# Kernel optimization log

Hardware: AMD Instinct MI355X
Metric: run time of the kernel (lower is better)

## Reference

```python
import jax, jax.numpy as jnp
import numpy as np

BS, S, DM, H = 4, 512, 512, 8
DK = DM // H
EPS = 1e-6


def setup_inputs() -> dict:
    key = jax.random.key(0)
    ks = jax.random.split(key, 11)
    sc = jnp.float32(0.02)  # small init so exp(q @ k^T) stays finite (no max-subtraction in original)
    return {
        "q": jax.random.normal(ks[0], (BS, S, DM), jnp.float32),
        "k": jax.random.normal(ks[1], (BS, S, DM), jnp.float32),
        "v": jax.random.normal(ks[2], (BS, S, DM), jnp.float32),
        "Wq": sc * jax.random.normal(ks[3], (DM, DM), jnp.float32),
        "bq": jnp.zeros((DM,), jnp.float32),
        "Wk": sc * jax.random.normal(ks[4], (DM, DM), jnp.float32),
        "bk": jnp.zeros((DM,), jnp.float32),
        "Wv": sc * jax.random.normal(ks[5], (DM, DM), jnp.float32),
        "bv": jnp.zeros((DM,), jnp.float32),
        "Wo": sc * jax.random.normal(ks[6], (DM, DM), jnp.float32),
        "bo": jnp.zeros((DM,), jnp.float32),
        "alpha": jnp.ones((DK,), jnp.float32),   # Norm.alpha over last dim (= d_k per head)
        "beta": jnp.zeros((DK,), jnp.float32),   # Norm.bias
    }


def reference(q, k, v, Wq, bq, Wk, bk, Wv, bv, Wo, bo, alpha, beta):
    # project and split heads: [bs, h, s, d_k]
    qh = (q @ Wq + bq).reshape(BS, S, H, DK).transpose(0, 2, 1, 3)
    kh = (k @ Wk + bk).reshape(BS, S, H, DK).transpose(0, 2, 1, 3)
    vh = (v @ Wv + bv).reshape(BS, S, H, DK).transpose(0, 2, 1, 3)

    # pairwise-batch exp scores: E[bq, bk, h, i, j] = exp(q[bq] @ k[bk]^T)
    E = jnp.exp(jnp.einsum('bhid,chjd->bchij', qh, kh))  # [BS, BS, H, S, S]
    # fenmu: sum over k-batch, each term scaled by sqrt(d_k) (as in original loop)
    fenmu = jnp.sqrt(jnp.float32(DK)) * E.sum(axis=1)     # [BS, H, S, S]
    # fenzi: same-batch exp scores (diagonal of pairwise tensor)
    fenzi = E[jnp.arange(BS), jnp.arange(BS)]             # [BS, H, S, S]
    R = fenzi / fenmu                                     # [BS, H, S, S]

    # per v-batch-entry score: score[bq, c] = R[bq] @ v[c]
    score = jnp.einsum('bhij,chjd->bchid', R, vh)         # [BS, BS, H, S, DK]
    sm = jax.nn.softmax(score, axis=-1)
    # Norm: torch.std is unbiased (ddof=1); eps added to std, not variance
    mu = sm.mean(axis=-1, keepdims=True)
    std = jnp.sqrt(sm.var(axis=-1, ddof=1, keepdims=True))
    ln = alpha * (sm - mu) / (std + EPS) + beta

    # output += LN(score) + q, accumulated over the v-batch loop (BS iterations)
    heads = ln.sum(axis=1) + jnp.float32(BS) * qh         # [BS, H, S, DK]
    concat = heads.transpose(0, 2, 1, 3).reshape(BS, S, DM)
    return concat @ Wo + bo
```

## Files before the change

### kernel.cpp

```cpp
#include <hip/hip_runtime.h>
#include <hip/hip_bf16.h>

#define BSZ 4
#define SEQ 512
#define DMODEL 512
#define NHEAD 8
#define DKH 64
#define EPSLN 1e-6f

typedef short bf16x8 __attribute__((ext_vector_type(8)));
typedef float f32x4 __attribute__((ext_vector_type(4)));

static __device__ __forceinline__ short f2bf(float x) {
  unsigned u = __builtin_bit_cast(unsigned, x);
  u = (u + 0x7FFFu + ((u >> 16) & 1u)) >> 16;
  return (short)u;
}
static __device__ __forceinline__ bf16x8 cvt8(float4 a, float4 b) {
  bf16x8 r;
  r[0] = f2bf(a.x); r[1] = f2bf(a.y); r[2] = f2bf(a.z); r[3] = f2bf(a.w);
  r[4] = f2bf(b.x); r[5] = f2bf(b.y); r[6] = f2bf(b.z); r[7] = f2bf(b.w);
  return r;
}
static __device__ __forceinline__ unsigned pk2(float a, float b) {
  return (unsigned)(unsigned short)f2bf(a) |
         ((unsigned)(unsigned short)f2bf(b) << 16);
}
static __device__ __forceinline__ void async_cp16(const void* g, void* l) {
  __builtin_amdgcn_global_load_lds(
      (const __attribute__((address_space(1))) unsigned int*)g,
      (__attribute__((address_space(3))) unsigned int*)l, 16, 0, 0);
}

__global__ __launch_bounds__(256) void cast3_kernel(
    const float* __restrict__ q, const float* __restrict__ k,
    const float* __restrict__ v, short* __restrict__ qb,
    short* __restrict__ kb, short* __restrict__ vb) {
  const float* s; short* d;
  switch (blockIdx.y) {
    case 0: s = q; d = qb; break;
    case 1: s = k; d = kb; break;
    default: s = v; d = vb; break;
  }
  const size_t idx = (size_t)blockIdx.x * 2048 + (size_t)threadIdx.x * 8;
  float4 a = *(const float4*)&s[idx];
  float4 b = *(const float4*)&s[idx + 4];
  *(bf16x8*)&d[idx] = cvt8(a, b);
}

__global__ __launch_bounds__(256) void wcast_kernel(
    const float* __restrict__ Wq, const float* __restrict__ Wk,
    const float* __restrict__ Wv, const float* __restrict__ Wo,
    short* __restrict__ Wqt, short* __restrict__ Wkt,
    short* __restrict__ Wvt, short* __restrict__ Wot) {
  __shared__ float T[64][65];
  const float* src; short* dst;
  switch (blockIdx.z) {
    case 0: src = Wq; dst = Wqt; break;
    case 1: src = Wk; dst = Wkt; break;
    case 2: src = Wv; dst = Wvt; break;
    default: src = Wo; dst = Wot; break;
  }
  const int k0 = blockIdx.x * 64, n0 = blockIdx.y * 64;
  const int tid = threadIdx.x;
  const int n4 = (tid & 15) * 4, kk = tid >> 4;
#pragma unroll
  for (int p = 0; p < 4; ++p) {
    float4 v = *(const float4*)&src[(size_t)(k0 + kk + p * 16) * DMODEL + n0 + n4];
    T[kk + p * 16][n4 + 0] = v.x;
    T[kk + p * 16][n4 + 1] = v.y;
    T[kk + p * 16][n4 + 2] = v.z;
    T[kk + p * 16][n4 + 3] = v.w;
  }
  __syncthreads();
  const int k4 = (tid & 15) * 4;
#pragma unroll
  for (int p = 0; p < 4; ++p) {
    const int nn = (tid >> 4) + p * 16;
    float x0 = T[k4 + 0][nn], x1 = T[k4 + 1][nn];
    float x2 = T[k4 + 2][nn], x3 = T[k4 + 3][nn];
    uint2 u; u.x = pk2(x0, x1); u.y = pk2(x2, x3);
    *(uint2*)&dst[(size_t)(n0 + nn) * DMODEL + k0 + k4] = u;
  }
}

__device__ __forceinline__ void gemm_body(
    const short* __restrict__ A, const short* __restrict__ Wt,
    const float* __restrict__ bias, void* __restrict__ out, int omode) {
  __shared__ short As[2][128 * 32];
  __shared__ short Bs[2][128 * 32];
  const int tid = threadIdx.x;
  const int w = tid >> 6, lane = tid & 63;
  const int l15 = lane & 15, q = lane >> 4;
  const int wm = w >> 1, wn = w & 1;
  const int bn = blockIdx.x * 128, bm = blockIdx.y * 128;
  const int wu = __builtin_amdgcn_readfirstlane(w);
  const int srow = wu * 16 + (lane >> 2);
  const int sch = lane & 3;

  f32x4 acc[4][4] = {};

#define GSTAGE(k0, buf)                                                      \
  {                                                                          \
    const short* ga0 = A + (size_t)(bm + srow) * 512 + (k0) + sch * 8;       \
    const short* ga1 = A + (size_t)(bm + srow + 64) * 512 + (k0) + sch * 8;  \
    const short* gb0 = Wt + (size_t)(bn + srow) * 512 + (k0) + sch * 8;      \
    const short* gb1 = Wt + (size_t)(bn + srow + 64) * 512 + (k0) + sch * 8; \
    async_cp16(ga0, &As[buf][wu * 512]);                                     \
    async_cp16(ga1, &As[buf][(4 + wu) * 512]);                               \
    async_cp16(gb0, &Bs[buf][wu * 512]);                                     \
    async_cp16(gb1, &Bs[buf][(4 + wu) * 512]);                               \
  }

  GSTAGE(0, 0);
  for (int ks = 0; ks < 16; ++ks) {
    __syncthreads();
    if (ks < 15) GSTAGE((ks + 1) * 32, (ks + 1) & 1);
    const short* a = As[ks & 1];
    const short* bsh = Bs[ks & 1];
    bf16x8 af[4], bfr[4];
#pragma unroll
    for (int mt = 0; mt < 4; ++mt)
      af[mt] = *(const bf16x8*)&a[(wm * 64 + mt * 16 + l15) * 32 + q * 8];
#pragma unroll
    for (int nt = 0; nt < 4; ++nt)
      bfr[nt] = *(const bf16x8*)&bsh[(wn * 64 + nt * 16 + l15) * 32 + q * 8];
#pragma unroll
    for (int mt = 0; mt < 4; ++mt)
#pragma unroll
      for (int nt = 0; nt < 4; ++nt)
        acc[mt][nt] = __builtin_amdgcn_mfma_f32_16x16x32_bf16(
            af[mt], bfr[nt], acc[mt][nt], 0, 0, 0);
  }
#undef GSTAGE

  float bv[4];
#pragma unroll
  for (int nt = 0; nt < 4; ++nt) bv[nt] = bias[bn + wn * 64 + nt * 16 + l15];
#pragma unroll
  for (int mt = 0; mt < 4; ++mt)
#pragma unroll
    for (int nt = 0; nt < 4; ++nt) {
      const int col = bn + wn * 64 + nt * 16 + l15;
#pragma unroll
      for (int r = 0; r < 4; ++r) {
        const int row = bm + wm * 64 + mt * 16 + q * 4 + r;
        const float val = acc[mt][nt][r] + bv[nt];
        if (omode == 0) {
          ((float*)out)[(size_t)row * 512 + col] = val;
        } else if (omode == 1) {
          ((short*)out)[(size_t)row * 512 + col] = f2bf(val);
        } else {
          const int cc = row >> 9, j = row & 511;
          const int hh = col >> 6, d = col & 63;
          ((short*)out)[(((size_t)(cc * 8 + hh) * 64 + d) << 9) + j] = f2bf(val);
        }
      }
    }
}

__global__ __launch_bounds__(256, 2) void proj_gemm(
    const short* qb, const short* kb, const short* vb,
    const short* Wqt, const short* Wkt, const short* Wvt,
    const float* bq, const float* bk, const float* bvs,
    float* Qp, short* Kb, short* Vt) {
  const short* A; const short* Wt; const float* bias; void* out; int omode;
  switch (blockIdx.z) {
    case 0: A = qb; Wt = Wqt; bias = bq; out = Qp; omode = 0; break;
    case 1: A = kb; Wt = Wkt; bias = bk; out = Kb; omode = 1; break;
    default: A = vb; Wt = Wvt; bias = bvs; out = Vt; omode = 2; break;
  }
  gemm_body(A, Wt, bias, out, omode);
}

__global__ __launch_bounds__(256, 2) void out_gemm(
    const short* Hc, const short* Wot, const float* bo, float* out) {
  gemm_body(Hc, Wot, bo, out, 0);
}

__global__ __launch_bounds__(256, 3) void attn2_kernel(
    const float* __restrict__ Qp, const short* __restrict__ Kb,
    const short* __restrict__ Vt, const float* __restrict__ alpha,
    const float* __restrict__ beta, short* __restrict__ Hc) {
  __shared__ __align__(16) short Stage[2][64 * 64];
  __shared__ __align__(16) short Rs[32][72];
  __shared__ __align__(16) float xch[16 * 128];

  const int it = blockIdx.x, h = blockIdx.y, b = blockIdx.z;
  const int i0 = it * 32;
  const int tid = threadIdx.x;
  const int w = tid >> 6, lane = tid & 63;
  const int l15 = lane & 15, q = lane >> 4;
  const int wi = w >> 1, wj = w & 1;
  const int wu = __builtin_amdgcn_readfirstlane(w);

  const float* qrow =
      Qp + (size_t)(b * SEQ + i0 + wi * 16 + l15) * DMODEL + h * DKH;
  const bf16x8 aq0 = cvt8(*(const float4*)(qrow + q * 8),
                          *(const float4*)(qrow + q * 8 + 4));
  const bf16x8 aq1 = cvt8(*(const float4*)(qrow + 32 + q * 8),
                          *(const float4*)(qrow + 32 + q * 8 + 4));

  const int srow0 = wu * 8 + (lane >> 3);
  const int scol = (lane & 7) ^ (lane >> 3);

  const short* kbase_h = Kb + h * DKH;
  const short* vbase_h = Vt + (((size_t)h * DKH) << 9);

#define STG(g0, rstride, buf)                                             \
  {                                                                       \
    async_cp16((g0) + (size_t)srow0 * (rstride) + scol * 8,               \
               &Stage[buf][wu * 512]);                                    \
    async_cp16((g0) + (size_t)(srow0 + 32) * (rstride) + scol * 8,        \
               &Stage[buf][(4 + wu) * 512]);                              \
  }

  f32x4 acc[4][4] = {};
  float sacc[2][4], ebb[2][4];

  STG(kbase_h, DMODEL, 0);

  for (int jt = 0; jt < 8; ++jt) {
    const int j0 = jt * 64;
    bf16x8 ar;
#pragma unroll
    for (int ph = 0; ph < 8; ++ph) {
      __syncthreads();
      const int buf = ph & 1, nbuf = buf ^ 1;
      if (ph < 3) {
        STG(kbase_h + ((size_t)((ph + 1) * SEQ) + j0) * DMODEL, DMODEL, nbuf);
      } else if (ph < 7) {
        const int cn = ph - 3;
        STG(vbase_h + (((size_t)(cn * NHEAD * DKH)) << 9) + j0, SEQ, nbuf);
      } else if (jt < 7) {
        STG(kbase_h + (size_t)(j0 + 64) * DMODEL, DMODEL, nbuf);
      }
      const short* S = Stage[buf];
      if (ph < 4) {
        if (ph == 0) {
#pragma unroll
          for (int t = 0; t < 2; ++t)
#pragma unroll
            for (int r = 0; r < 4; ++r) sacc[t][r] = 0.0f;
        }
#pragma unroll
        for (int ntl = 0; ntl < 2; ++ntl) {
          const int row = (wj * 2 + ntl) * 16 + l15;
          const int p0 = q ^ (l15 & 7);
          bf16x8 b0 = *(const bf16x8*)&S[row * 64 + p0 * 8];
          bf16x8 b1 = *(const bf16x8*)&S[row * 64 + (p0 ^ 4) * 8];
          f32x4 s = {};
          s = __builtin_amdgcn_mfma_f32_16x16x32_bf16(aq0, b0, s, 0, 0, 0);
          s = __builtin_amdgcn_mfma_f32_16x16x32_bf16(aq1, b1, s, 0, 0, 0);
#pragma unroll
          for (int r = 0; r < 4; ++r) {
            const float e = __expf(s[r]);
            sacc[ntl][r] += e;
            if (ph == b) ebb[ntl][r] = e;
          }
        }
        if (ph == 3) {
#pragma unroll
          for (int ntl = 0; ntl < 2; ++ntl)
#pragma unroll
            for (int r = 0; r < 4; ++r)
              Rs[wi * 16 + q * 4 + r][(wj * 2 + ntl) * 16 + l15] =
                  f2bf(ebb[ntl][r] / (8.0f * sacc[ntl][r]));
        }
      } else {
        if (ph == 4) ar = *(const bf16x8*)&Rs[wi * 16 + l15][wj * 32 + q * 8];
#pragma unroll
        for (int nt = 0; nt < 4; ++nt) {
          const int row = nt * 16 + l15;
          const int pb = (wj * 4 + q) ^ (l15 & 7);
          bf16x8 bv = *(const bf16x8*)&S[row * 64 + pb * 8];
          acc[ph - 4][nt] = __builtin_amdgcn_mfma_f32_16x16x32_bf16(
              ar, bv, acc[ph - 4][nt], 0, 0, 0);
        }
      }
    }
  }
#undef STG

#pragma unroll
  for (int c = 0; c < BSZ; ++c) {
    if (wj == 1) {
#pragma unroll
      for (int nt = 0; nt < 4; ++nt)
#pragma unroll
        for (int r = 0; r < 4; ++r)
          xch[(nt * 4 + r) * 128 + wi * 64 + lane] = acc[c][nt][r];
    }
    __syncthreads();
    if (wj == 0) {
#pragma unroll
      for (int nt = 0; nt < 4; ++nt)
#pragma unroll
        for (int r = 0; r < 4; ++r)
          acc[c][nt][r] += xch[(nt * 4 + r) * 128 + wi * 64 + lane];
    }
    __syncthreads();
  }

  if (wj == 0) {
    float al[4], be[4];
#pragma unroll
    for (int nt = 0; nt < 4; ++nt) {
      al[nt] = alpha[nt * 16 + l15];
      be[nt] = beta[nt * 16 + l15];
    }
    float hacc[4][4] = {};
#pragma unroll
    for (int c = 0; c < BSZ; ++c) {
#pragma unroll
      for (int r = 0; r < 4; ++r) {
        float e0 = __expf(acc[c][0][r]), e1 = __expf(acc[c][1][r]);
        float e2 = __expf(acc[c][2][r]), e3 = __expf(acc[c][3][r]);
        float es = e0 + e1 + e2 + e3;
#pragma unroll
        for (int m = 8; m >= 1; m >>= 1) es += __shfl_xor(es, m);
        const float inv = 1.0f / es;
        const float d0 = e0 * inv - 0.015625f, d1 = e1 * inv - 0.015625f;
        const float d2 = e2 * inv - 0.015625f, d3 = e3 * inv - 0.015625f;
        float sq = d0 * d0 + d1 * d1 + d2 * d2 + d3 * d3;
#pragma unroll
        for (int m = 8; m >= 1; m >>= 1) sq += __shfl_xor(sq, m);
        const float rs = 1.0f / (sqrtf(sq * (1.0f / 63.0f)) + EPSLN);
        hacc[r][0] += al[0] * d0 * rs + be[0];
        hacc[r][1] += al[1] * d1 * rs + be[1];
        hacc[r][2] += al[2] * d2 * rs + be[2];
        hacc[r][3] += al[3] * d3 * rs + be[3];
      }
    }
#pragma unroll
    for (int r = 0; r < 4; ++r) {
      const size_t rowoff =
          (size_t)(b * SEQ + i0 + wi * 16 + q * 4 + r) * DMODEL + h * DKH;
#pragma unroll
      for (int nt = 0; nt < 4; ++nt) {
        const int d = nt * 16 + l15;
        const float o = hacc[r][nt] + 4.0f * Qp[rowoff + d];
        Hc[rowoff + d] = f2bf(o);
      }
    }
  }
}

extern "C" void kernel_launch(void* const* d_in, const int* in_sizes, int n_in,
                              void* d_out, int out_size, void* d_ws,
                              size_t ws_size, hipStream_t stream) {
  (void)in_sizes; (void)n_in; (void)out_size; (void)ws_size;
  const float* q = (const float*)d_in[0];
  const float* k = (const float*)d_in[1];
  const float* v = (const float*)d_in[2];
  const float* Wq = (const float*)d_in[3];
  const float* bq = (const float*)d_in[4];
  const float* Wk = (const float*)d_in[5];
  const float* bk = (const float*)d_in[6];
  const float* Wv = (const float*)d_in[7];
  const float* bv = (const float*)d_in[8];
  const float* Wo = (const float*)d_in[9];
  const float* bo = (const float*)d_in[10];
  const float* alpha = (const float*)d_in[11];
  const float* beta = (const float*)d_in[12];
  float* out = (float*)d_out;

  char* wsb = (char*)d_ws;
  short* qb = (short*)(wsb);
  short* kb = (short*)(wsb + (2u << 20));
  short* vb = (short*)(wsb + (4u << 20));
  float* Qp = (float*)(wsb + (6u << 20));
  short* Kb = (short*)(wsb + (10u << 20));
  short* Vtg = (short*)(wsb + (12u << 20));
  short* Hc = (short*)(wsb + (14u << 20));
  short* Wqt = (short*)(wsb + (16u << 20));
  short* Wkt = (short*)(wsb + (16u << 20) + (512u << 10));
  short* Wvt = (short*)(wsb + (17u << 20));
  short* Wot = (short*)(wsb + (17u << 20) + (512u << 10));

  cast3_kernel<<<dim3(512, 3), 256, 0, stream>>>(q, k, v, qb, kb, vb);
  wcast_kernel<<<dim3(8, 8, 4), 256, 0, stream>>>(Wq, Wk, Wv, Wo,
                                                  Wqt, Wkt, Wvt, Wot);
  proj_gemm<<<dim3(4, 16, 3), 256, 0, stream>>>(qb, kb, vb, Wqt, Wkt, Wvt,
                                                bq, bk, bv, Qp, Kb, Vtg);
  attn2_kernel<<<dim3(16, 8, 4), 256, 0, stream>>>(Qp, Kb, Vtg, alpha, beta,
                                                   Hc);
  out_gemm<<<dim3(4, 16), 256, 0, stream>>>(Hc, Wot, bo, out);
}
```

Measured before the change: 161.0 us.

## Merge cast kernels and stage two K/V tiles per barrier in attention

The activation cast and weight transpose-cast kernels become one launch, dispatched by block index, which saves a kernel launch. In the attention kernel each pipeline phase now loads and consumes two 64x64 tiles instead of one. That halves the number of __syncthreads per j-tile, from 8 to 4, and doubles the staging LDS. The larger LDS footprint may lower occupancy under the 3-blocks-per-CU launch bound.

```diff
diff --git a/kernel.cpp b/kernel.cpp
--- a/kernel.cpp
+++ b/kernel.cpp
@@ -32,45 +32,49 @@
       (__attribute__((address_space(3))) unsigned int*)l, 16, 0, 0);
 }
 
-__global__ __launch_bounds__(256) void cast3_kernel(
+__global__ __launch_bounds__(256) void prep_kernel(
     const float* __restrict__ q, const float* __restrict__ k,
     const float* __restrict__ v, short* __restrict__ qb,
-    short* __restrict__ kb, short* __restrict__ vb) {
-  const float* s; short* d;
-  switch (blockIdx.y) {
-    case 0: s = q; d = qb; break;
-    case 1: s = k; d = kb; break;
-    default: s = v; d = vb; break;
-  }
-  const size_t idx = (size_t)blockIdx.x * 2048 + (size_t)threadIdx.x * 8;
-  float4 a = *(const float4*)&s[idx];
-  float4 b = *(const float4*)&s[idx + 4];
-  *(bf16x8*)&d[idx] = cvt8(a, b);
-}
-
-__global__ __launch_bounds__(256) void wcast_kernel(
+    short* __restrict__ kb, short* __restrict__ vb,
     const float* __restrict__ Wq, const float* __restrict__ Wk,
     const float* __restrict__ Wv, const float* __restrict__ Wo,
     short* __restrict__ Wqt, short* __restrict__ Wkt,
     short* __restrict__ Wvt, short* __restrict__ Wot) {
   __shared__ float T[64][65];
+  const int bx = blockIdx.x;
+  if (bx < 1536) {
+    const int which = bx >> 9, blk = bx & 511;
+    const float* s; short* d;
+    switch (which) {
+      case 0: s = q; d = qb; break;
+      case 1: s = k; d = kb; break;
+      default: s = v; d = vb; break;
+    }
+    const size_t idx = (size_t)blk * 2048 + (size_t)threadIdx.x * 8;
+    float4 a = *(const float4*)&s[idx];
+    float4 b = *(const float4*)&s[idx + 4];
+    *(bf16x8*)&d[idx] = cvt8(a, b);
+    return;
+  }
+  const int r = bx - 1536;
+  const int mat = r >> 6, m = r & 63;
+  const int k0 = (m & 7) * 64, n0 = (m >> 3) * 64;
   const float* src; short* dst;
-  switch (blockIdx.z) {
+  switch (mat) {
     case 0: src = Wq; dst = Wqt; break;
     case 1: src = Wk; dst = Wkt; break;
     case 2: src = Wv; dst = Wvt; break;
     default: src = Wo; dst = Wot; break;
   }
-  const int k0 = blockIdx.x * 64, n0 = blockIdx.y * 64;
   const int tid = threadIdx.x;
   const int n4 = (tid & 15) * 4, kk = tid >> 4;
 #pragma unroll
   for (int p = 0; p < 4; ++p) {
-    float4 v = *(const float4*)&src[(size_t)(k0 + kk + p * 16) * DMODEL + n0 + n4];
-    T[kk + p * 16][n4 + 0] = v.x;
-    T[kk + p * 16][n4 + 1] = v.y;
-    T[kk + p * 16][n4 + 2] = v.z;
-    T[kk + p * 16][n4 + 3] = v.w;
+    float4 w4 = *(const float4*)&src[(size_t)(k0 + kk + p * 16) * DMODEL + n0 + n4];
+    T[kk + p * 16][n4 + 0] = w4.x;
+    T[kk + p * 16][n4 + 1] = w4.y;
+    T[kk + p * 16][n4 + 2] = w4.z;
+    T[kk + p * 16][n4 + 3] = w4.w;
   }
   __syncthreads();
   const int k4 = (tid & 15) * 4;
@@ -182,7 +186,7 @@
     const float* __restrict__ Qp, const short* __restrict__ Kb,
     const short* __restrict__ Vt, const float* __restrict__ alpha,
     const float* __restrict__ beta, short* __restrict__ Hc) {
-  __shared__ __align__(16) short Stage[2][64 * 64];
+  __shared__ __align__(16) short Stage[2][2 * 4096];
   __shared__ __align__(16) short Rs[32][72];
   __shared__ __align__(16) float xch[16 * 128];
 
@@ -207,59 +211,71 @@
   const short* kbase_h = Kb + h * DKH;
   const short* vbase_h = Vt + (((size_t)h * DKH) << 9);
 
-#define STG(g0, rstride, buf)                                             \
+#define STG1(g0, rs, buf, tslot)                                          \
   {                                                                       \
-    async_cp16((g0) + (size_t)srow0 * (rstride) + scol * 8,               \
-               &Stage[buf][wu * 512]);                                    \
-    async_cp16((g0) + (size_t)(srow0 + 32) * (rstride) + scol * 8,        \
-               &Stage[buf][(4 + wu) * 512]);                              \
-  }
+    async_cp16((g0) + (size_t)srow0 * (rs) + scol * 8,                    \
+               &Stage[buf][(tslot) * 4096 + wu * 512]);                   \
+    async_cp16((g0) + (size_t)(srow0 + 32) * (rs) + scol * 8,             \
+               &Stage[buf][(tslot) * 4096 + (4 + wu) * 512]);             \
+  }
+#define KTILE(c, j0) (kbase_h + ((size_t)((c) * SEQ) + (j0)) * DMODEL)
+#define VTILE(c, j0) (vbase_h + (((size_t)((c) * NHEAD * DKH)) << 9) + (j0))
 
   f32x4 acc[4][4] = {};
   float sacc[2][4], ebb[2][4];
 
-  STG(kbase_h, DMODEL, 0);
+  STG1(KTILE(0, 0), DMODEL, 0, 0);
+  STG1(KTILE(1, 0), DMODEL, 0, 1);
 
   for (int jt = 0; jt < 8; ++jt) {
     const int j0 = jt * 64;
     bf16x8 ar;
 #pragma unroll
-    for (int ph = 0; ph < 8; ++ph) {
+    for (int ph2 = 0; ph2 < 4; ++ph2) {
       __syncthreads();
-      const int buf = ph & 1, nbuf = buf ^ 1;
-      if (ph < 3) {
-        STG(kbase_h + ((size_t)((ph + 1) * SEQ) + j0) * DMODEL, DMODEL, nbuf);
-      } else if (ph < 7) {
-        const int cn = ph - 3;
-        STG(vbase_h + (((size_t)(cn * NHEAD * DKH)) << 9) + j0, SEQ, nbuf);
+      const int buf = ph2 & 1, nbuf = buf ^ 1;
+      if (ph2 == 0) {
+        STG1(KTILE(2, j0), DMODEL, nbuf, 0);
+        STG1(KTILE(3, j0), DMODEL, nbuf, 1);
+      } else if (ph2 == 1) {
+        STG1(VTILE(0, j0), SEQ, nbuf, 0);
+        STG1(VTILE(1, j0), SEQ, nbuf, 1);
+      } else if (ph2 == 2) {
+        STG1(VTILE(2, j0), SEQ, nbuf, 0);
+        STG1(VTILE(3, j0), SEQ, nbuf, 1);
       } else if (jt < 7) {
-        STG(kbase_h + (size_t)(j0 + 64) * DMODEL, DMODEL, nbuf);
+        STG1(KTILE(0, j0 + 64), DMODEL, nbuf, 0);
+        STG1(KTILE(1, j0 + 64), DMODEL, nbuf, 1);
       }
-      const short* S = Stage[buf];
-      if (ph < 4) {
-        if (ph == 0) {
+      if (ph2 < 2) {
+        if (ph2 == 0) {
 #pragma unroll
           for (int t = 0; t < 2; ++t)
 #pragma unroll
-            for (int r = 0; r < 4; ++r) sacc[t][r] = 0.0f;
+            for (int r = 0; r < 4; ++r) { sacc[t][r] = 0.0f; ebb[t][r] = 0.0f; }
         }
 #pragma unroll
-        for (int ntl = 0; ntl < 2; ++ntl) {
-          const int row = (wj * 2 + ntl) * 16 + l15;
-          const int p0 = q ^ (l15 & 7);
-          bf16x8 b0 = *(const bf16x8*)&S[row * 64 + p0 * 8];
-          bf16x8 b1 = *(const bf16x8*)&S[row * 64 + (p0 ^ 4) * 8];
-          f32x4 s = {};
-          s = __builtin_amdgcn_mfma_f32_16x16x32_bf16(aq0, b0, s, 0, 0, 0);
-          s = __builtin_amdgcn_mfma_f32_16x16x32_bf16(aq1, b1, s, 0, 0, 0);
-#pragma unroll
-          for (int r = 0; r < 4; ++r) {
-            const float e = __expf(s[r]);
-            sacc[ntl][r] += e;
-            if (ph == b) ebb[ntl][r] = e;
+        for (int ct = 0; ct < 2; ++ct) {
+          const int c = ph2 * 2 + ct;
+          const short* S = &Stage[buf][ct * 4096];
+#pragma unroll
+          for (int ntl = 0; ntl < 2; ++ntl) {
+            const int row = (wj * 2 + ntl) * 16 + l15;
+            const int p0 = q ^ (l15 & 7);
+            bf16x8 b0 = *(const bf16x8*)&S[row * 64 + p0 * 8];
+            bf16x8 b1 = *(const bf16x8*)&S[row * 64 + (p0 ^ 4) * 8];
+            f32x4 s = {};
+            s = __builtin_amdgcn_mfma_f32_16x16x32_bf16(aq0, b0, s, 0, 0, 0);
+            s = __builtin_amdgcn_mfma_f32_16x16x32_bf16(aq1, b1, s, 0, 0, 0);
+#pragma unroll
+            for (int r = 0; r < 4; ++r) {
+              const float e = __expf(s[r]);
+              sacc[ntl][r] += e;
+              ebb[ntl][r] = (c == b) ? e : ebb[ntl][r];
+            }
           }
         }
-        if (ph == 3) {
+        if (ph2 == 1) {
 #pragma unroll
           for (int ntl = 0; ntl < 2; ++ntl)
 #pragma unroll
@@ -268,19 +284,26 @@
                   f2bf(ebb[ntl][r] / (8.0f * sacc[ntl][r]));
         }
       } else {
-        if (ph == 4) ar = *(const bf16x8*)&Rs[wi * 16 + l15][wj * 32 + q * 8];
-#pragma unroll
-        for (int nt = 0; nt < 4; ++nt) {
-          const int row = nt * 16 + l15;
-          const int pb = (wj * 4 + q) ^ (l15 & 7);
-          bf16x8 bv = *(const bf16x8*)&S[row * 64 + pb * 8];
-          acc[ph - 4][nt] = __builtin_amdgcn_mfma_f32_16x16x32_bf16(
-              ar, bv, acc[ph - 4][nt], 0, 0, 0);
+        if (ph2 == 2) ar = *(const bf16x8*)&Rs[wi * 16 + l15][wj * 32 + q * 8];
+#pragma unroll
+        for (int ct = 0; ct < 2; ++ct) {
+          const int c = (ph2 - 2) * 2 + ct;
+          const short* S = &Stage[buf][ct * 4096];
+#pragma unroll
+          for (int nt = 0; nt < 4; ++nt) {
+            const int row = nt * 16 + l15;
+            const int pb = (wj * 4 + q) ^ (l15 & 7);
+            bf16x8 bv = *(const bf16x8*)&S[row * 64 + pb * 8];
+            acc[c][nt] = __builtin_amdgcn_mfma_f32_16x16x32_bf16(
+                ar, bv, acc[c][nt], 0, 0, 0);
+          }
         }
       }
     }
   }
-#undef STG
+#undef STG1
+#undef KTILE
+#undef VTILE
 
 #pragma unroll
   for (int c = 0; c < BSZ; ++c) {
@@ -378,9 +401,9 @@
   short* Wvt = (short*)(wsb + (17u << 20));
   short* Wot = (short*)(wsb + (17u << 20) + (512u << 10));
 
-  cast3_kernel<<<dim3(512, 3), 256, 0, stream>>>(q, k, v, qb, kb, vb);
-  wcast_kernel<<<dim3(8, 8, 4), 256, 0, stream>>>(Wq, Wk, Wv, Wo,
-                                                  Wqt, Wkt, Wvt, Wot);
+  prep_kernel<<<dim3(1792), 256, 0, stream>>>(q, k, v, qb, kb, vb,
+                                              Wq, Wk, Wv, Wo,
+                                              Wqt, Wkt, Wvt, Wot);
   proj_gemm<<<dim3(4, 16, 3), 256, 0, stream>>>(qb, kb, vb, Wqt, Wkt, Wvt,
                                                 bq, bk, bv, Qp, Kb, Vtg);
   attn2_kernel<<<dim3(16, 8, 4), 256, 0, stream>>>(Qp, Kb, Vtg, alpha, beta,
```

After: 150.2 us. -6.7%, faster.
